# Kernel tuning notes

Hardware: AMD Instinct MI355X
Metric: run time of the kernel (lower is better)

Reference implementation:

```python
import jax, jax.numpy as jnp
import numpy as np

N_NODES = 50000
N_EDGES = 800000
HIDDEN = 64
DEPTH = 3
NUM_GRAPHS = 256
NUM_CLASSES = 1
BN_EPS = 1e-5


def setup_inputs() -> dict:
    key = jax.random.key(0)
    ks = jax.random.split(key, 12)
    x = jax.random.normal(ks[0], (N_NODES, HIDDEN), dtype=jnp.float32)
    edge_index = jax.random.randint(ks[1], (2, N_EDGES), 0, N_NODES, dtype=jnp.int32)
    batch = jnp.sort(jax.random.randint(ks[2], (N_NODES,), 0, NUM_GRAPHS, dtype=jnp.int32))
    s = 1.0 / np.sqrt(HIDDEN)
    W1 = jax.random.uniform(ks[3], (DEPTH, HIDDEN, HIDDEN), jnp.float32, -s, s)
    b1 = jax.random.uniform(ks[4], (DEPTH, HIDDEN), jnp.float32, -s, s)
    W2 = jax.random.uniform(ks[5], (DEPTH, HIDDEN, HIDDEN), jnp.float32, -s, s)
    b2 = jax.random.uniform(ks[6], (DEPTH, HIDDEN), jnp.float32, -s, s)
    gamma = jnp.ones((DEPTH, HIDDEN), jnp.float32)
    beta = jnp.zeros((DEPTH, HIDDEN), jnp.float32)
    Wf = jax.random.uniform(ks[7], (HIDDEN, NUM_CLASSES), jnp.float32, -s, s)
    bf = jax.random.uniform(ks[8], (NUM_CLASSES,), jnp.float32, -s, s)
    return {"x": x, "edge_index": edge_index, "batch": batch,
            "W1": W1, "b1": b1, "W2": W2, "b2": b2,
            "gamma": gamma, "beta": beta, "Wf": Wf, "bf": bf}


def reference(x, edge_index, batch, W1, b1, W2, b2, gamma, beta, Wf, bf):
    src, dst = edge_index[0], edge_index[1]
    for i in range(DEPTH):
        # GINConv: (1+eps)*x + scatter-add of neighbor features (eps=0)
        agg = jnp.zeros_like(x).at[dst].add(x[src])
        h = x + agg
        h = jax.nn.relu(h @ W1[i] + b1[i])
        h = jax.nn.relu(h @ W2[i] + b2[i])
        # BatchNorm over node dimension (training-mode batch stats)
        mean = h.mean(axis=0)
        var = ((h - mean) ** 2).mean(axis=0)
        h = (h - mean) * jax.lax.rsqrt(var + BN_EPS) * gamma[i] + beta[i]
        x = jax.nn.relu(h)
    pooled = jax.ops.segment_sum(x, batch, num_segments=NUM_GRAPHS)  # [G, H]
    return pooled @ Wf + bf
```

## Files before the change

kernel.cpp:

```cpp
#include <hip/hip_runtime.h>

#define HIDDEN_C 64
#define NCHUNK 256

typedef __attribute__((ext_vector_type(8))) short bf16x8;
typedef __attribute__((ext_vector_type(8))) unsigned short u16x8;
typedef __attribute__((ext_vector_type(4))) float f32x4;

__device__ __forceinline__ float4 f4zero() { return make_float4(0.f, 0.f, 0.f, 0.f); }

__device__ __forceinline__ unsigned short f2bf(float f) {
    unsigned u = __float_as_uint(f);
    u += 0x7FFF + ((u >> 16) & 1);
    return (unsigned short)(u >> 16);
}
__device__ __forceinline__ float bf2f(unsigned short h) {
    return __uint_as_float(((unsigned)h) << 16);
}

__device__ __forceinline__ int swz_idx(int row, int k) {
    return row * 64 + ((((k >> 3) ^ (row & 7)) << 3) | (k & 7));
}

__global__ __launch_bounds__(256) void k_blocksum(const int* __restrict__ deg,
                                                  int* __restrict__ partial, int n) {
    int base = blockIdx.x * 1024 + threadIdx.x * 4;
    int s = 0;
#pragma unroll
    for (int k = 0; k < 4; ++k) {
        int i = base + k;
        if (i < n) s += deg[i];
    }
    __shared__ int red[256];
    red[threadIdx.x] = s;
    __syncthreads();
    for (int d = 128; d > 0; d >>= 1) {
        if (threadIdx.x < d) red[threadIdx.x] += red[threadIdx.x + d];
        __syncthreads();
    }
    if (threadIdx.x == 0) partial[blockIdx.x] = red[0];
}

__global__ __launch_bounds__(256) void k_scanpartial(int* __restrict__ partial,
                                                     int* __restrict__ last_slot,
                                                     int nBlocks, int nE) {
    __shared__ int buf[256];
    int tid = threadIdx.x;
    int v = (tid < nBlocks) ? partial[tid] : 0;
    buf[tid] = v;
    __syncthreads();
    for (int d = 1; d < 256; d <<= 1) {
        int t = (tid >= d) ? buf[tid - d] : 0;
        __syncthreads();
        buf[tid] += t;
        __syncthreads();
    }
    if (tid < nBlocks) partial[tid] = buf[tid] - v;
    if (tid == 0) last_slot[0] = nE;
}

__global__ __launch_bounds__(256) void k_writeptr(const int* __restrict__ deg,
                                                  const int* __restrict__ partial,
                                                  int* __restrict__ outp, int n) {
    int tid = threadIdx.x;
    int base = blockIdx.x * 1024 + tid * 4;
    int d[4];
    int s = 0;
#pragma unroll
    for (int k = 0; k < 4; ++k) {
        int i = base + k;
        d[k] = (i < n) ? deg[i] : 0;
        s += d[k];
    }
    __shared__ int buf[256];
    buf[tid] = s;
    __syncthreads();
    for (int dd = 1; dd < 256; dd <<= 1) {
        int t = (tid >= dd) ? buf[tid - dd] : 0;
        __syncthreads();
        buf[tid] += t;
        __syncthreads();
    }
    int off = partial[blockIdx.x] + buf[tid] - s;
#pragma unroll
    for (int k = 0; k < 4; ++k) {
        int i = base + k;
        if (i < n) {
            outp[i] = off;
            off += d[k];
        }
    }
}

__global__ __launch_bounds__(256) void k_bcount(const int* __restrict__ dst,
                                                int* __restrict__ cnt,
                                                int nE, int chunkSz, int nBuckets) {
    __shared__ int h[1024];
    int c = blockIdx.x, tid = threadIdx.x;
    for (int i = tid; i < nBuckets; i += 256) h[i] = 0;
    __syncthreads();
    int beg = c * chunkSz;
    int end = beg + chunkSz; if (end > nE) end = nE;
    int e = beg + tid;
    for (; e + 256 < end; e += 512) {
        int d0 = dst[e];
        int d1 = dst[e + 256];
        atomicAdd(&h[d0 >> 6], 1);
        atomicAdd(&h[d1 >> 6], 1);
    }
    if (e < end) atomicAdd(&h[dst[e] >> 6], 1);
    __syncthreads();
    for (int i = tid; i < nBuckets; i += 256) cnt[i * NCHUNK + c] = h[i];
}

__global__ __launch_bounds__(256) void k_bscatter(const int* __restrict__ src,
                                                  const int* __restrict__ dst,
                                                  const int* __restrict__ eoff,
                                                  unsigned* __restrict__ ebuf,
                                                  int nE, int chunkSz, int nBuckets) {
    __shared__ int cur[1024];
    int c = blockIdx.x, tid = threadIdx.x;
    for (int i = tid; i < nBuckets; i += 256) cur[i] = eoff[i * NCHUNK + c];
    __syncthreads();
    int beg = c * chunkSz;
    int end = beg + chunkSz; if (end > nE) end = nE;
    int e = beg + tid;
    for (; e + 256 < end; e += 512) {
        int d0 = dst[e];
        int d1 = dst[e + 256];
        int s0 = src[e];
        int s1 = src[e + 256];
        int p0 = atomicAdd(&cur[d0 >> 6], 1);
        int p1 = atomicAdd(&cur[d1 >> 6], 1);
        ebuf[p0] = ((unsigned)(d0 & 63) << 16) | (unsigned)s0;
        ebuf[p1] = ((unsigned)(d1 & 63) << 16) | (unsigned)s1;
    }
    if (e < end) {
        int d = dst[e];
        int pos = atomicAdd(&cur[d >> 6], 1);
        ebuf[pos] = ((unsigned)(d & 63) << 16) | (unsigned)src[e];
    }
}

__global__ __launch_bounds__(256) void k_bfill(const unsigned* __restrict__ ebuf,
                                               const int* __restrict__ eoff,
                                               int* __restrict__ rowptr,
                                               int* __restrict__ col,
                                               int nNodes, int nE, int nBuckets) {
    __shared__ int deg[64], cur[64];
    int b = blockIdx.x, tid = threadIdx.x;
    int lo = eoff[b * NCHUNK];
    int hi = (b + 1 < nBuckets) ? eoff[(b + 1) * NCHUNK] : nE;
    if (tid < 64) deg[tid] = 0;
    __syncthreads();
    for (int e = lo + tid; e < hi; e += 256) atomicAdd(&deg[ebuf[e] >> 16], 1);
    __syncthreads();
    if (tid < 64) {
        int d = deg[tid];
        int s = d;
        for (int o = 1; o < 64; o <<= 1) {
            int t = __shfl_up(s, o, 64);
            if (tid >= o) s += t;
        }
        int st = s - d;
        cur[tid] = lo + st;
        int node = b * 64 + tid;
        if (node < nNodes) rowptr[node] = lo + st;
    }
    __syncthreads();
    for (int e = lo + tid; e < hi; e += 256) {
        unsigned pk = ebuf[e];
        int pos = atomicAdd(&cur[pk >> 16], 1);
        col[pos] = (int)(pk & 0xFFFFu);
    }
}

__global__ __launch_bounds__(256) void k_wprep(const float* __restrict__ W1,
                                               const float* __restrict__ W2,
                                               unsigned short* __restrict__ wt) {
    __shared__ unsigned short s[8192];
    int b = blockIdx.x;
    int layer = b >> 1;
    const float* src = ((b & 1) ? W2 : W1) + (size_t)layer * 4096;
    int tid = threadIdx.x;
    int k = tid >> 2;
    int f0 = (tid & 3) * 16;
    const float* srcp = src + k * 64 + f0;
#pragma unroll
    for (int j4 = 0; j4 < 4; ++j4) {
        float4 wv = *(const float4*)(srcp + j4 * 4);
        float c[4] = {wv.x, wv.y, wv.z, wv.w};
        int f = f0 + j4 * 4;
#pragma unroll
        for (int j = 0; j < 4; ++j) {
            unsigned short h = f2bf(c[j]);
            int ix = swz_idx(f + j, k);
            s[ix] = h;
            s[4096 + ix] = f2bf(c[j] - bf2f(h));
        }
    }
    __syncthreads();
    uint4* dst = (uint4*)(wt + (size_t)b * 8192);
    const uint4* sp = (const uint4*)s;
#pragma unroll
    for (int it = 0; it < 4; ++it) dst[it * 256 + tid] = sp[it * 256 + tid];
}

__global__ __launch_bounds__(256) void k_statred(const float* __restrict__ pstat,
                                                 float* __restrict__ stats, int nb) {
    int j = blockIdx.x;
    int tid = threadIdx.x;
    float s = 0.f;
    for (int b = tid; b < nb; b += 256) s += pstat[(size_t)b * 128 + j];
    __shared__ float red[256];
    red[tid] = s;
    __syncthreads();
    for (int d = 128; d > 0; d >>= 1) {
        if (tid < d) red[tid] += red[tid + d];
        __syncthreads();
    }
    if (tid == 0) stats[j] = red[0];
}

template <bool DOBN>
__global__ __launch_bounds__(256) void k_aggbn(const float4* __restrict__ x4,
                                               const int* __restrict__ rowptr,
                                               const int* __restrict__ col,
                                               const float* __restrict__ stats,
                                               const float* __restrict__ gamma,
                                               const float* __restrict__ beta,
                                               float4* __restrict__ h4,
                                               int nNodes, float invN) {
    int wid = threadIdx.x >> 6;
    int lane = threadIdx.x & 63;
    int grp = lane >> 4;
    int l16 = lane & 15;
    int n = blockIdx.x * 4 + wid;
    if (n >= nNodes) return;

    float4 sc = make_float4(1.f, 1.f, 1.f, 1.f);
    float4 sh = f4zero();
    if (DOBN) {
        float4 s  = ((const float4*)stats)[l16];
        float4 q  = ((const float4*)stats)[16 + l16];
        float4 ga = ((const float4*)gamma)[l16];
        float4 be = ((const float4*)beta)[l16];
        float m;
        m = s.x * invN; sc.x = ga.x * rsqrtf(q.x * invN - m * m + 1e-5f); sh.x = be.x - m * sc.x;
        m = s.y * invN; sc.y = ga.y * rsqrtf(q.y * invN - m * m + 1e-5f); sh.y = be.y - m * sc.y;
        m = s.z * invN; sc.z = ga.z * rsqrtf(q.z * invN - m * m + 1e-5f); sh.z = be.z - m * sc.z;
        m = s.w * invN; sc.w = ga.w * rsqrtf(q.w * invN - m * m + 1e-5f); sh.w = be.w - m * sc.w;
    }

    float4 acc = f4zero();
    {
        float4 v = x4[(size_t)n * 16 + l16];
        if (DOBN) {
            v.x = fmaxf(fmaf(v.x, sc.x, sh.x), 0.f);
            v.y = fmaxf(fmaf(v.y, sc.y, sh.y), 0.f);
            v.z = fmaxf(fmaf(v.z, sc.z, sh.z), 0.f);
            v.w = fmaxf(fmaf(v.w, sc.w, sh.w), 0.f);
        }
        if (grp == 0) acc = v;
    }

    int lo = rowptr[n], hi = rowptr[n + 1];
    int e = lo;
    for (; e + 8 <= hi; e += 8) {
        int i0 = col[e + grp];
        int i1 = col[e + 4 + grp];
        float4 v0 = x4[(size_t)i0 * 16 + l16];
        float4 v1 = x4[(size_t)i1 * 16 + l16];
        if (DOBN) {
            v0.x = fmaxf(fmaf(v0.x, sc.x, sh.x), 0.f);
            v0.y = fmaxf(fmaf(v0.y, sc.y, sh.y), 0.f);
            v0.z = fmaxf(fmaf(v0.z, sc.z, sh.z), 0.f);
            v0.w = fmaxf(fmaf(v0.w, sc.w, sh.w), 0.f);
            v1.x = fmaxf(fmaf(v1.x, sc.x, sh.x), 0.f);
            v1.y = fmaxf(fmaf(v1.y, sc.y, sh.y), 0.f);
            v1.z = fmaxf(fmaf(v1.z, sc.z, sh.z), 0.f);
            v1.w = fmaxf(fmaf(v1.w, sc.w, sh.w), 0.f);
        }
        acc.x += v0.x + v1.x; acc.y += v0.y + v1.y;
        acc.z += v0.z + v1.z; acc.w += v0.w + v1.w;
    }
    for (; e < hi; e += 4) {
        int ee = e + grp;
        bool ok = ee < hi;
        int idx = col[ok ? ee : (hi - 1)];
        float4 v = x4[(size_t)idx * 16 + l16];
        if (DOBN) {
            v.x = fmaxf(fmaf(v.x, sc.x, sh.x), 0.f);
            v.y = fmaxf(fmaf(v.y, sc.y, sh.y), 0.f);
            v.z = fmaxf(fmaf(v.z, sc.z, sh.z), 0.f);
            v.w = fmaxf(fmaf(v.w, sc.w, sh.w), 0.f);
        }
        if (ok) {
            acc.x += v.x; acc.y += v.y; acc.z += v.z; acc.w += v.w;
        }
    }

    acc.x += __shfl_xor(acc.x, 16, 64); acc.y += __shfl_xor(acc.y, 16, 64);
    acc.z += __shfl_xor(acc.z, 16, 64); acc.w += __shfl_xor(acc.w, 16, 64);
    acc.x += __shfl_xor(acc.x, 32, 64); acc.y += __shfl_xor(acc.y, 32, 64);
    acc.z += __shfl_xor(acc.z, 32, 64); acc.w += __shfl_xor(acc.w, 32, 64);

    if (lane < 16) h4[(size_t)n * 16 + l16] = acc;
}

__global__ __launch_bounds__(256, 5) void k_mlp(const float* __restrict__ h_in,
                                                float* __restrict__ h_out,
                                                const unsigned short* __restrict__ wt1,
                                                const float* __restrict__ b1,
                                                const unsigned short* __restrict__ wt2,
                                                const float* __restrict__ b2,
                                                float* __restrict__ pstat,
                                                int nNodes) {
    __shared__ __align__(16) unsigned short smem16[16384];
    unsigned short* sA_hi = smem16;
    unsigned short* sA_lo = smem16 + 4096;
    unsigned short* sW_hi = smem16 + 8192;
    unsigned short* sW_lo = smem16 + 12288;

    int tid = threadIdx.x;
    int n0 = blockIdx.x * 64;
    int lane = tid & 63;
    int w = tid >> 6;
    int lr = lane & 15;
    int q = lane >> 4;
    int r0 = w * 16;

    uint4 w2r[4];
#pragma unroll
    for (int it = 0; it < 4; ++it) w2r[it] = ((const uint4*)wt2)[it * 256 + tid];

#pragma unroll
    for (int it = 0; it < 2; ++it) {
        int idx = it * 256 + tid;
        int row = idx >> 3, ch = idx & 7;
        float4 v0 = f4zero(), v1 = f4zero();
        if (n0 + row < nNodes) {
            const float4* p = (const float4*)(h_in + (size_t)(n0 + row) * 64 + ch * 8);
            v0 = p[0]; v1 = p[1];
        }
        float f[8] = {v0.x, v0.y, v0.z, v0.w, v1.x, v1.y, v1.z, v1.w};
        u16x8 hv, lv;
#pragma unroll
        for (int j = 0; j < 8; ++j) {
            unsigned short h = f2bf(f[j]);
            hv[j] = h;
            lv[j] = f2bf(f[j] - bf2f(h));
        }
        int off = row * 64 + ((ch ^ (row & 7)) << 3);
        *(u16x8*)(sA_hi + off) = hv;
        *(u16x8*)(sA_lo + off) = lv;
    }
    {
        uint4* d = (uint4*)sW_hi;
        const uint4* s = (const uint4*)wt1;
#pragma unroll
        for (int it = 0; it < 4; ++it) d[it * 256 + tid] = s[it * 256 + tid];
    }
    __syncthreads();

    f32x4 acc[4];

#define GEMM_SPLIT(BIAS)                                                         \
    {                                                                            \
        int rowA = r0 + lr;                                                      \
        const unsigned short* pah = sA_hi + rowA * 64;                           \
        const unsigned short* pal = sA_lo + rowA * 64;                           \
        int sr = rowA & 7;                                                       \
        bf16x8 ah0 = *(const bf16x8*)(pah + ((q ^ sr) << 3));                    \
        bf16x8 ah1 = *(const bf16x8*)(pah + (((4 + q) ^ sr) << 3));              \
        bf16x8 al0 = *(const bf16x8*)(pal + ((q ^ sr) << 3));                    \
        bf16x8 al1 = *(const bf16x8*)(pal + (((4 + q) ^ sr) << 3));              \
        _Pragma("unroll")                                                        \
        for (int ct = 0; ct < 4; ++ct) {                                         \
            int f = ct * 16 + lr;                                                \
            const unsigned short* pbh = sW_hi + f * 64;                          \
            const unsigned short* pbl = sW_lo + f * 64;                          \
            int sf = f & 7;                                                      \
            bf16x8 bh0 = *(const bf16x8*)(pbh + ((q ^ sf) << 3));                \
            bf16x8 bh1 = *(const bf16x8*)(pbh + (((4 + q) ^ sf) << 3));          \
            bf16x8 bl0 = *(const bf16x8*)(pbl + ((q ^ sf) << 3));                \
            bf16x8 bl1 = *(const bf16x8*)(pbl + (((4 + q) ^ sf) << 3));          \
            float bias = BIAS[f];                                                \
            f32x4 c = {bias, bias, bias, bias};                                  \
            c = __builtin_amdgcn_mfma_f32_16x16x32_bf16(al0, bh0, c, 0, 0, 0);   \
            c = __builtin_amdgcn_mfma_f32_16x16x32_bf16(al1, bh1, c, 0, 0, 0);   \
            c = __builtin_amdgcn_mfma_f32_16x16x32_bf16(ah0, bl0, c, 0, 0, 0);   \
            c = __builtin_amdgcn_mfma_f32_16x16x32_bf16(ah1, bl1, c, 0, 0, 0);   \
            c = __builtin_amdgcn_mfma_f32_16x16x32_bf16(ah0, bh0, c, 0, 0, 0);   \
            c = __builtin_amdgcn_mfma_f32_16x16x32_bf16(ah1, bh1, c, 0, 0, 0);   \
            acc[ct] = c;                                                         \
        }                                                                        \
    }

    GEMM_SPLIT(b1)

    __syncthreads();

#pragma unroll
    for (int ct = 0; ct < 4; ++ct) {
        int f = ct * 16 + lr;
#pragma unroll
        for (int rg = 0; rg < 4; ++rg) {
            int row = r0 + q * 4 + rg;
            float v = fmaxf(acc[ct][rg], 0.f);
            unsigned short h = f2bf(v);
            int ix = swz_idx(row, f);
            sA_hi[ix] = h;
            sA_lo[ix] = f2bf(v - bf2f(h));
        }
    }
    {
        uint4* d = (uint4*)sW_hi;
#pragma unroll
        for (int it = 0; it < 4; ++it) d[it * 256 + tid] = w2r[it];
    }
    __syncthreads();

    GEMM_SPLIT(b2)

    __syncthreads();
#undef GEMM_SPLIT

    float* sS = (float*)sW_hi;
    float* sQ = sS + 256;

#pragma unroll
    for (int ct = 0; ct < 4; ++ct) {
        int f = ct * 16 + lr;
        float sp = 0.f, qp = 0.f;
#pragma unroll
        for (int rg = 0; rg < 4; ++rg) {
            int row = r0 + q * 4 + rg;
            float v = fmaxf(acc[ct][rg], 0.f);
            if (n0 + row < nNodes) {
                h_out[(size_t)(n0 + row) * 64 + f] = v;
                sp += v;
                qp += v * v;
            }
        }
        sp += __shfl_xor(sp, 16, 64); qp += __shfl_xor(qp, 16, 64);
        sp += __shfl_xor(sp, 32, 64); qp += __shfl_xor(qp, 32, 64);
        if (q == 0) {
            sS[w * 64 + f] = sp;
            sQ[w * 64 + f] = qp;
        }
    }
    __syncthreads();
    if (tid < 128) {
        float v;
        if (tid < 64)
            v = sS[tid] + sS[64 + tid] + sS[128 + tid] + sS[192 + tid];
        else {
            int f = tid - 64;
            v = sQ[f] + sQ[64 + f] + sQ[128 + f] + sQ[192 + f];
        }
        pstat[(size_t)blockIdx.x * 128 + tid] = v;
    }
}

__device__ __forceinline__ int lower_bound_dev(const int* a, int n, int key) {
    int lo = 0, hi = n;
    while (lo < hi) {
        int mid = (lo + hi) >> 1;
        if (a[mid] < key) lo = mid + 1; else hi = mid;
    }
    return lo;
}

__global__ __launch_bounds__(256) void k_pool(const float4* __restrict__ x4,
                                              const int* __restrict__ batch,
                                              const float* __restrict__ stats,
                                              const float* __restrict__ gamma,
                                              const float* __restrict__ beta,
                                              const float* __restrict__ Wf,
                                              const float* __restrict__ bf,
                                              float* __restrict__ out,
                                              int nNodes, float invN) {
    int wid = threadIdx.x >> 6;
    int lane = threadIdx.x & 63;
    int grp = lane >> 4;
    int l16 = lane & 15;
    int g = blockIdx.x * 4 + wid;

    float4 sc, sh;
    {
        float4 s  = ((const float4*)stats)[l16];
        float4 q  = ((const float4*)stats)[16 + l16];
        float4 ga = ((const float4*)gamma)[l16];
        float4 be = ((const float4*)beta)[l16];
        float m;
        m = s.x * invN; sc.x = ga.x * rsqrtf(q.x * invN - m * m + 1e-5f); sh.x = be.x - m * sc.x;
        m = s.y * invN; sc.y = ga.y * rsqrtf(q.y * invN - m * m + 1e-5f); sh.y = be.y - m * sc.y;
        m = s.z * invN; sc.z = ga.z * rsqrtf(q.z * invN - m * m + 1e-5f); sh.z = be.z - m * sc.z;
        m = s.w * invN; sc.w = ga.w * rsqrtf(q.w * invN - m * m + 1e-5f); sh.w = be.w - m * sc.w;
    }

    int lo = lower_bound_dev(batch, nNodes, g);
    int hi = lower_bound_dev(batch, nNodes, g + 1);

    float4 acc = f4zero();
    for (int r = lo + grp; r < hi; r += 4) {
        float4 v = x4[(size_t)r * 16 + l16];
        acc.x += fmaxf(fmaf(v.x, sc.x, sh.x), 0.f);
        acc.y += fmaxf(fmaf(v.y, sc.y, sh.y), 0.f);
        acc.z += fmaxf(fmaf(v.z, sc.z, sh.z), 0.f);
        acc.w += fmaxf(fmaf(v.w, sc.w, sh.w), 0.f);
    }
    acc.x += __shfl_xor(acc.x, 16, 64); acc.y += __shfl_xor(acc.y, 16, 64);
    acc.z += __shfl_xor(acc.z, 16, 64); acc.w += __shfl_xor(acc.w, 16, 64);
    acc.x += __shfl_xor(acc.x, 32, 64); acc.y += __shfl_xor(acc.y, 32, 64);
    acc.z += __shfl_xor(acc.z, 32, 64); acc.w += __shfl_xor(acc.w, 32, 64);

    float4 wf = ((const float4*)Wf)[l16];
    float p = acc.x * wf.x + acc.y * wf.y + acc.z * wf.z + acc.w * wf.w;
    p += __shfl_xor(p, 1, 64);
    p += __shfl_xor(p, 2, 64);
    p += __shfl_xor(p, 4, 64);
    p += __shfl_xor(p, 8, 64);
    if (lane == 0) out[g] = p + bf[0];
}

extern "C" void kernel_launch(void* const* d_in, const int* in_sizes, int n_in,
                              void* d_out, int out_size, void* d_ws, size_t ws_size,
                              hipStream_t stream) {
    const float* x_in  = (const float*)d_in[0];
    const int*   ei    = (const int*)d_in[1];
    const int*   batch = (const int*)d_in[2];
    const float* W1    = (const float*)d_in[3];
    const float* b1    = (const float*)d_in[4];
    const float* W2    = (const float*)d_in[5];
    const float* b2    = (const float*)d_in[6];
    const float* gamma = (const float*)d_in[7];
    const float* beta  = (const float*)d_in[8];
    const float* Wf    = (const float*)d_in[9];
    const float* bf    = (const float*)d_in[10];

    const int nNodes = in_sizes[0] / HIDDEN_C;
    const int nE = in_sizes[1] / 2;
    const int* src = ei;
    const int* dst = ei + nE;

    const int nBuckets = (nNodes + 63) / 64;
    const int nTot = nBuckets * NCHUNK;
    const int chunkSz = (nE + NCHUNK - 1) / NCHUNK;
    const int scanBlocks = (nTot + 1023) / 1024;
    const float invN = 1.f / (float)nNodes;

    const size_t NB = (size_t)nNodes * HIDDEN_C * sizeof(float);
    char* ws = (char*)d_ws;
    float*    bufA    = (float*)ws;
    float*    bufB    = (float*)(ws + NB);
    float*    stats   = (float*)(ws + 2 * NB);
    unsigned short* wtbuf = (unsigned short*)(ws + 2 * NB + 4096);
    float*    pstat   = (float*)(ws + 2 * NB + 4096 + 98304);
    int*      rowptr  = (int*)((char*)pstat + 409600);
    int*      partial = rowptr + nNodes + 64;
    int*      col     = partial + 256;
    unsigned* ebuf    = (unsigned*)bufB;
    int*      cnt     = (int*)((char*)bufB + (size_t)nE * 4);
    int*      eoff    = cnt + nTot + 64;

    const int mlpGrid = nBuckets;
    const int aggGrid = (nNodes + 3) / 4;

    k_wprep<<<6, 256, 0, stream>>>(W1, W2, wtbuf);
    k_bcount<<<NCHUNK, 256, 0, stream>>>(dst, cnt, nE, chunkSz, nBuckets);
    k_blocksum<<<scanBlocks, 256, 0, stream>>>(cnt, partial, nTot);
    k_scanpartial<<<1, 256, 0, stream>>>(partial, rowptr + nNodes, scanBlocks, nE);
    k_writeptr<<<scanBlocks, 256, 0, stream>>>(cnt, partial, eoff, nTot);
    k_bscatter<<<NCHUNK, 256, 0, stream>>>(src, dst, eoff, ebuf, nE, chunkSz, nBuckets);
    k_bfill<<<nBuckets, 256, 0, stream>>>(ebuf, eoff, rowptr, col, nNodes, nE, nBuckets);

    const float* prev_h = x_in;
    float* cur = bufA;
    for (int i = 0; i < 3; ++i) {
        if (i == 0) {
            k_aggbn<false><<<aggGrid, 256, 0, stream>>>((const float4*)prev_h, rowptr, col,
                                                        nullptr, nullptr, nullptr,
                                                        (float4*)cur, nNodes, invN);
        } else {
            k_aggbn<true><<<aggGrid, 256, 0, stream>>>((const float4*)prev_h, rowptr, col,
                                                       stats + (size_t)(i - 1) * 128,
                                                       gamma + (size_t)(i - 1) * 64,
                                                       beta + (size_t)(i - 1) * 64,
                                                       (float4*)cur, nNodes, invN);
        }
        k_mlp<<<mlpGrid, 256, 0, stream>>>(cur, cur,
                                           wtbuf + (size_t)(2 * i) * 8192, b1 + (size_t)i * 64,
                                           wtbuf + (size_t)(2 * i + 1) * 8192, b2 + (size_t)i * 64,
                                           pstat, nNodes);
        k_statred<<<128, 256, 0, stream>>>(pstat, stats + (size_t)i * 128, nBuckets);
        prev_h = cur;
        cur = (cur == bufA) ? bufB : bufA;
    }

    k_pool<<<64, 256, 0, stream>>>((const float4*)prev_h, batch,
                                   stats + 256, gamma + 128, beta + 128,
                                   Wf, bf, (float*)d_out, nNodes, invN);
}
```

Before: 212.8 us.

## Fuse neighbor aggregation and BN into the MLP kernel per layer

```diff
diff --git a/kernel.cpp b/kernel.cpp
--- a/kernel.cpp
+++ b/kernel.cpp
@@ -223,99 +223,19 @@
 }
 
 template <bool DOBN>
-__global__ __launch_bounds__(256) void k_aggbn(const float4* __restrict__ x4,
-                                               const int* __restrict__ rowptr,
-                                               const int* __restrict__ col,
-                                               const float* __restrict__ stats,
-                                               const float* __restrict__ gamma,
-                                               const float* __restrict__ beta,
-                                               float4* __restrict__ h4,
-                                               int nNodes, float invN) {
-    int wid = threadIdx.x >> 6;
-    int lane = threadIdx.x & 63;
-    int grp = lane >> 4;
-    int l16 = lane & 15;
-    int n = blockIdx.x * 4 + wid;
-    if (n >= nNodes) return;
-
-    float4 sc = make_float4(1.f, 1.f, 1.f, 1.f);
-    float4 sh = f4zero();
-    if (DOBN) {
-        float4 s  = ((const float4*)stats)[l16];
-        float4 q  = ((const float4*)stats)[16 + l16];
-        float4 ga = ((const float4*)gamma)[l16];
-        float4 be = ((const float4*)beta)[l16];
-        float m;
-        m = s.x * invN; sc.x = ga.x * rsqrtf(q.x * invN - m * m + 1e-5f); sh.x = be.x - m * sc.x;
-        m = s.y * invN; sc.y = ga.y * rsqrtf(q.y * invN - m * m + 1e-5f); sh.y = be.y - m * sc.y;
-        m = s.z * invN; sc.z = ga.z * rsqrtf(q.z * invN - m * m + 1e-5f); sh.z = be.z - m * sc.z;
-        m = s.w * invN; sc.w = ga.w * rsqrtf(q.w * invN - m * m + 1e-5f); sh.w = be.w - m * sc.w;
-    }
-
-    float4 acc = f4zero();
-    {
-        float4 v = x4[(size_t)n * 16 + l16];
-        if (DOBN) {
-            v.x = fmaxf(fmaf(v.x, sc.x, sh.x), 0.f);
-            v.y = fmaxf(fmaf(v.y, sc.y, sh.y), 0.f);
-            v.z = fmaxf(fmaf(v.z, sc.z, sh.z), 0.f);
-            v.w = fmaxf(fmaf(v.w, sc.w, sh.w), 0.f);
-        }
-        if (grp == 0) acc = v;
-    }
-
-    int lo = rowptr[n], hi = rowptr[n + 1];
-    int e = lo;
-    for (; e + 8 <= hi; e += 8) {
-        int i0 = col[e + grp];
-        int i1 = col[e + 4 + grp];
-        float4 v0 = x4[(size_t)i0 * 16 + l16];
-        float4 v1 = x4[(size_t)i1 * 16 + l16];
-        if (DOBN) {
-            v0.x = fmaxf(fmaf(v0.x, sc.x, sh.x), 0.f);
-            v0.y = fmaxf(fmaf(v0.y, sc.y, sh.y), 0.f);
-            v0.z = fmaxf(fmaf(v0.z, sc.z, sh.z), 0.f);
-            v0.w = fmaxf(fmaf(v0.w, sc.w, sh.w), 0.f);
-            v1.x = fmaxf(fmaf(v1.x, sc.x, sh.x), 0.f);
-            v1.y = fmaxf(fmaf(v1.y, sc.y, sh.y), 0.f);
-            v1.z = fmaxf(fmaf(v1.z, sc.z, sh.z), 0.f);
-            v1.w = fmaxf(fmaf(v1.w, sc.w, sh.w), 0.f);
-        }
-        acc.x += v0.x + v1.x; acc.y += v0.y + v1.y;
-        acc.z += v0.z + v1.z; acc.w += v0.w + v1.w;
-    }
-    for (; e < hi; e += 4) {
-        int ee = e + grp;
-        bool ok = ee < hi;
-        int idx = col[ok ? ee : (hi - 1)];
-        float4 v = x4[(size_t)idx * 16 + l16];
-        if (DOBN) {
-            v.x = fmaxf(fmaf(v.x, sc.x, sh.x), 0.f);
-            v.y = fmaxf(fmaf(v.y, sc.y, sh.y), 0.f);
-            v.z = fmaxf(fmaf(v.z, sc.z, sh.z), 0.f);
-            v.w = fmaxf(fmaf(v.w, sc.w, sh.w), 0.f);
-        }
-        if (ok) {
-            acc.x += v.x; acc.y += v.y; acc.z += v.z; acc.w += v.w;
-        }
-    }
-
-    acc.x += __shfl_xor(acc.x, 16, 64); acc.y += __shfl_xor(acc.y, 16, 64);
-    acc.z += __shfl_xor(acc.z, 16, 64); acc.w += __shfl_xor(acc.w, 16, 64);
-    acc.x += __shfl_xor(acc.x, 32, 64); acc.y += __shfl_xor(acc.y, 32, 64);
-    acc.z += __shfl_xor(acc.z, 32, 64); acc.w += __shfl_xor(acc.w, 32, 64);
-
-    if (lane < 16) h4[(size_t)n * 16 + l16] = acc;
-}
-
-__global__ __launch_bounds__(256, 5) void k_mlp(const float* __restrict__ h_in,
-                                                float* __restrict__ h_out,
-                                                const unsigned short* __restrict__ wt1,
-                                                const float* __restrict__ b1,
-                                                const unsigned short* __restrict__ wt2,
-                                                const float* __restrict__ b2,
-                                                float* __restrict__ pstat,
-                                                int nNodes) {
+__global__ __launch_bounds__(256, 5) void k_layer(const float4* __restrict__ x4,
+                                                  const int* __restrict__ rowptr,
+                                                  const int* __restrict__ col,
+                                                  const float* __restrict__ stats,
+                                                  const float* __restrict__ gamma,
+                                                  const float* __restrict__ beta,
+                                                  const unsigned short* __restrict__ wt1,
+                                                  const float* __restrict__ b1,
+                                                  const unsigned short* __restrict__ wt2,
+                                                  const float* __restrict__ b2,
+                                                  float* __restrict__ pstat,
+                                                  float* __restrict__ h_out,
+                                                  int nNodes, float invN) {
     __shared__ __align__(16) unsigned short smem16[16384];
     unsigned short* sA_hi = smem16;
     unsigned short* sA_lo = smem16 + 4096;
@@ -329,38 +249,92 @@
     int lr = lane & 15;
     int q = lane >> 4;
     int r0 = w * 16;
+    int grp = lane >> 4;
+    int l16 = lane & 15;
 
     uint4 w2r[4];
 #pragma unroll
     for (int it = 0; it < 4; ++it) w2r[it] = ((const uint4*)wt2)[it * 256 + tid];
 
-#pragma unroll
-    for (int it = 0; it < 2; ++it) {
-        int idx = it * 256 + tid;
-        int row = idx >> 3, ch = idx & 7;
-        float4 v0 = f4zero(), v1 = f4zero();
-        if (n0 + row < nNodes) {
-            const float4* p = (const float4*)(h_in + (size_t)(n0 + row) * 64 + ch * 8);
-            v0 = p[0]; v1 = p[1];
-        }
-        float f[8] = {v0.x, v0.y, v0.z, v0.w, v1.x, v1.y, v1.z, v1.w};
-        u16x8 hv, lv;
-#pragma unroll
-        for (int j = 0; j < 8; ++j) {
-            unsigned short h = f2bf(f[j]);
-            hv[j] = h;
-            lv[j] = f2bf(f[j] - bf2f(h));
-        }
-        int off = row * 64 + ((ch ^ (row & 7)) << 3);
-        *(u16x8*)(sA_hi + off) = hv;
-        *(u16x8*)(sA_lo + off) = lv;
-    }
     {
         uint4* d = (uint4*)sW_hi;
         const uint4* s = (const uint4*)wt1;
 #pragma unroll
         for (int it = 0; it < 4; ++it) d[it * 256 + tid] = s[it * 256 + tid];
     }
+
+    float4 sc = make_float4(1.f, 1.f, 1.f, 1.f);
+    float4 sh = f4zero();
+    if (DOBN) {
+        float4 s  = ((const float4*)stats)[l16];
+        float4 qv = ((const float4*)stats)[16 + l16];
+        float4 ga = ((const float4*)gamma)[l16];
+        float4 be = ((const float4*)beta)[l16];
+        float m;
+        m = s.x * invN; sc.x = ga.x * rsqrtf(qv.x * invN - m * m + 1e-5f); sh.x = be.x - m * sc.x;
+        m = s.y * invN; sc.y = ga.y * rsqrtf(qv.y * invN - m * m + 1e-5f); sh.y = be.y - m * sc.y;
+        m = s.z * invN; sc.z = ga.z * rsqrtf(qv.z * invN - m * m + 1e-5f); sh.z = be.z - m * sc.z;
+        m = s.w * invN; sc.w = ga.w * rsqrtf(qv.w * invN - m * m + 1e-5f); sh.w = be.w - m * sc.w;
+    }
+
+#define APPLYBN(V)                                          \
+    if (DOBN) {                                             \
+        V.x = fmaxf(fmaf(V.x, sc.x, sh.x), 0.f);            \
+        V.y = fmaxf(fmaf(V.y, sc.y, sh.y), 0.f);            \
+        V.z = fmaxf(fmaf(V.z, sc.z, sh.z), 0.f);            \
+        V.w = fmaxf(fmaf(V.w, sc.w, sh.w), 0.f);            \
+    }
+
+    for (int i = 0; i < 16; ++i) {
+        int rloc = r0 + i;
+        int n = n0 + rloc;
+        float4 acc = f4zero();
+        if (n < nNodes) {
+            if (grp == 0) {
+                float4 v = x4[(size_t)n * 16 + l16];
+                APPLYBN(v)
+                acc = v;
+            }
+            int lo = rowptr[n], hi = rowptr[n + 1];
+            int e = lo;
+            for (; e + 8 <= hi; e += 8) {
+                int i0 = col[e + grp];
+                int i1 = col[e + 4 + grp];
+                float4 v0 = x4[(size_t)i0 * 16 + l16];
+                float4 v1 = x4[(size_t)i1 * 16 + l16];
+                APPLYBN(v0)
+                APPLYBN(v1)
+                acc.x += v0.x + v1.x; acc.y += v0.y + v1.y;
+                acc.z += v0.z + v1.z; acc.w += v0.w + v1.w;
+            }
+            for (; e < hi; e += 4) {
+                int ee = e + grp;
+                bool ok = ee < hi;
+                int idx = col[ok ? ee : (hi - 1)];
+                float4 v = x4[(size_t)idx * 16 + l16];
+                APPLYBN(v)
+                if (ok) {
+                    acc.x += v.x; acc.y += v.y; acc.z += v.z; acc.w += v.w;
+                }
+            }
+        }
+        acc.x += __shfl_xor(acc.x, 16, 64); acc.y += __shfl_xor(acc.y, 16, 64);
+        acc.z += __shfl_xor(acc.z, 16, 64); acc.w += __shfl_xor(acc.w, 16, 64);
+        acc.x += __shfl_xor(acc.x, 32, 64); acc.y += __shfl_xor(acc.y, 32, 64);
+        acc.z += __shfl_xor(acc.z, 32, 64); acc.w += __shfl_xor(acc.w, 32, 64);
+
+        if (lane < 16) {
+            ushort4 hv, lv;
+            hv.x = f2bf(acc.x); lv.x = f2bf(acc.x - bf2f(hv.x));
+            hv.y = f2bf(acc.y); lv.y = f2bf(acc.y - bf2f(hv.y));
+            hv.z = f2bf(acc.z); lv.z = f2bf(acc.z - bf2f(hv.z));
+            hv.w = f2bf(acc.w); lv.w = f2bf(acc.w - bf2f(hv.w));
+            int ix = rloc * 64 + ((((l16 >> 1) ^ (rloc & 7)) << 3) | ((l16 & 1) << 2));
+            *(ushort4*)(sA_hi + ix) = hv;
+            *(ushort4*)(sA_lo + ix) = lv;
+        }
+    }
+#undef APPLYBN
     __syncthreads();
 
     f32x4 acc[4];
@@ -565,8 +539,7 @@
     int*      cnt     = (int*)((char*)bufB + (size_t)nE * 4);
     int*      eoff    = cnt + nTot + 64;
 
-    const int mlpGrid = nBuckets;
-    const int aggGrid = (nNodes + 3) / 4;
+    const int layerGrid = nBuckets;
 
     k_wprep<<<6, 256, 0, stream>>>(W1, W2, wtbuf);
     k_bcount<<<NCHUNK, 256, 0, stream>>>(dst, cnt, nE, chunkSz, nBuckets);
@@ -580,20 +553,17 @@
     float* cur = bufA;
     for (int i = 0; i < 3; ++i) {
         if (i == 0) {
-            k_aggbn<false><<<aggGrid, 256, 0, stream>>>((const float4*)prev_h, rowptr, col,
-                                                        nullptr, nullptr, nullptr,
-                                                        (float4*)cur, nNodes, invN);
+            k_layer<false><<<layerGrid, 256, 0, stream>>>((const float4*)prev_h, rowptr, col,
+                nullptr, nullptr, nullptr,
+                wtbuf, b1, wtbuf + 8192, b2,
+                pstat, cur, nNodes, invN);
         } else {
-            k_aggbn<true><<<aggGrid, 256, 0, stream>>>((const float4*)prev_h, rowptr, col,
-                                                       stats + (size_t)(i - 1) * 128,
-                                                       gamma + (size_t)(i - 1) * 64,
-                                                       beta + (size_t)(i - 1) * 64,
-                                                       (float4*)cur, nNodes, invN);
-        }
-        k_mlp<<<mlpGrid, 256, 0, stream>>>(cur, cur,
-                                           wtbuf + (size_t)(2 * i) * 8192, b1 + (size_t)i * 64,
-                                           wtbuf + (size_t)(2 * i + 1) * 8192, b2 + (size_t)i * 64,
-                                           pstat, nNodes);
+            k_layer<true><<<layerGrid, 256, 0, stream>>>((const float4*)prev_h, rowptr, col,
+                stats + (size_t)(i - 1) * 128, gamma + (size_t)(i - 1) * 64, beta + (size_t)(i - 1) * 64,
+                wtbuf + (size_t)(2 * i) * 8192, b1 + (size_t)i * 64,
+                wtbuf + (size_t)(2 * i + 1) * 8192, b2 + (size_t)i * 64,
+                pstat, cur, nNodes, invN);
+        }
         k_statred<<<128, 256, 0, stream>>>(pstat, stats + (size_t)i * 128, nBuckets);
         prev_h = cur;
         cur = (cur == bufA) ? bufB : bufA;
```

Result: slower. 251.7 us (+18.3%).

## Store node feature buffers in fp16 to halve gather and stream bandwidth

Applied to the files above, without the earlier changes.

```diff
diff --git a/kernel.cpp b/kernel.cpp
--- a/kernel.cpp
+++ b/kernel.cpp
@@ -17,9 +17,31 @@
 __device__ __forceinline__ float bf2f(unsigned short h) {
     return __uint_as_float(((unsigned)h) << 16);
 }
+__device__ __forceinline__ unsigned short f2h(float f) {
+    _Float16 h = (_Float16)f;
+    unsigned short u;
+    __builtin_memcpy(&u, &h, 2);
+    return u;
+}
+__device__ __forceinline__ float h2f(unsigned short u) {
+    _Float16 h;
+    __builtin_memcpy(&h, &u, 2);
+    return (float)h;
+}
 
 __device__ __forceinline__ int swz_idx(int row, int k) {
     return row * 64 + ((((k >> 3) ^ (row & 7)) << 3) | (k & 7));
+}
+
+__global__ __launch_bounds__(256) void k_xcvt(const float4* __restrict__ in,
+                                              ushort4* __restrict__ out, int n4) {
+    int i = blockIdx.x * 256 + threadIdx.x;
+    if (i < n4) {
+        float4 v = in[i];
+        ushort4 o;
+        o.x = f2h(v.x); o.y = f2h(v.y); o.z = f2h(v.z); o.w = f2h(v.w);
+        out[i] = o;
+    }
 }
 
 __global__ __launch_bounds__(256) void k_blocksum(const int* __restrict__ deg,
@@ -223,13 +245,13 @@
 }
 
 template <bool DOBN>
-__global__ __launch_bounds__(256) void k_aggbn(const float4* __restrict__ x4,
+__global__ __launch_bounds__(256) void k_aggbn(const unsigned short* __restrict__ x16,
                                                const int* __restrict__ rowptr,
                                                const int* __restrict__ col,
                                                const float* __restrict__ stats,
                                                const float* __restrict__ gamma,
                                                const float* __restrict__ beta,
-                                               float4* __restrict__ h4,
+                                               unsigned short* __restrict__ hout,
                                                int nNodes, float invN) {
     int wid = threadIdx.x >> 6;
     int lane = threadIdx.x & 63;
@@ -252,15 +274,22 @@
         m = s.w * invN; sc.w = ga.w * rsqrtf(q.w * invN - m * m + 1e-5f); sh.w = be.w - m * sc.w;
     }
 
+#define LOADROW(IDX, V)                                                      \
+    {                                                                        \
+        ushort4 uv = *(const ushort4*)(x16 + (size_t)(IDX) * 64 + l16 * 4);  \
+        V.x = h2f(uv.x); V.y = h2f(uv.y); V.z = h2f(uv.z); V.w = h2f(uv.w);  \
+        if (DOBN) {                                                          \
+            V.x = fmaxf(fmaf(V.x, sc.x, sh.x), 0.f);                         \
+            V.y = fmaxf(fmaf(V.y, sc.y, sh.y), 0.f);                         \
+            V.z = fmaxf(fmaf(V.z, sc.z, sh.z), 0.f);                         \
+            V.w = fmaxf(fmaf(V.w, sc.w, sh.w), 0.f);                         \
+        }                                                                    \
+    }
+
     float4 acc = f4zero();
     {
-        float4 v = x4[(size_t)n * 16 + l16];
-        if (DOBN) {
-            v.x = fmaxf(fmaf(v.x, sc.x, sh.x), 0.f);
-            v.y = fmaxf(fmaf(v.y, sc.y, sh.y), 0.f);
-            v.z = fmaxf(fmaf(v.z, sc.z, sh.z), 0.f);
-            v.w = fmaxf(fmaf(v.w, sc.w, sh.w), 0.f);
-        }
+        float4 v;
+        LOADROW(n, v)
         if (grp == 0) acc = v;
     }
 
@@ -269,18 +298,9 @@
     for (; e + 8 <= hi; e += 8) {
         int i0 = col[e + grp];
         int i1 = col[e + 4 + grp];
-        float4 v0 = x4[(size_t)i0 * 16 + l16];
-        float4 v1 = x4[(size_t)i1 * 16 + l16];
-        if (DOBN) {
-            v0.x = fmaxf(fmaf(v0.x, sc.x, sh.x), 0.f);
-            v0.y = fmaxf(fmaf(v0.y, sc.y, sh.y), 0.f);
-            v0.z = fmaxf(fmaf(v0.z, sc.z, sh.z), 0.f);
-            v0.w = fmaxf(fmaf(v0.w, sc.w, sh.w), 0.f);
-            v1.x = fmaxf(fmaf(v1.x, sc.x, sh.x), 0.f);
-            v1.y = fmaxf(fmaf(v1.y, sc.y, sh.y), 0.f);
-            v1.z = fmaxf(fmaf(v1.z, sc.z, sh.z), 0.f);
-            v1.w = fmaxf(fmaf(v1.w, sc.w, sh.w), 0.f);
-        }
+        float4 v0, v1;
+        LOADROW(i0, v0)
+        LOADROW(i1, v1)
         acc.x += v0.x + v1.x; acc.y += v0.y + v1.y;
         acc.z += v0.z + v1.z; acc.w += v0.w + v1.w;
     }
@@ -288,28 +308,28 @@
         int ee = e + grp;
         bool ok = ee < hi;
         int idx = col[ok ? ee : (hi - 1)];
-        float4 v = x4[(size_t)idx * 16 + l16];
-        if (DOBN) {
-            v.x = fmaxf(fmaf(v.x, sc.x, sh.x), 0.f);
-            v.y = fmaxf(fmaf(v.y, sc.y, sh.y), 0.f);
-            v.z = fmaxf(fmaf(v.z, sc.z, sh.z), 0.f);
-            v.w = fmaxf(fmaf(v.w, sc.w, sh.w), 0.f);
-        }
+        float4 v;
+        LOADROW(idx, v)
         if (ok) {
             acc.x += v.x; acc.y += v.y; acc.z += v.z; acc.w += v.w;
         }
     }
+#undef LOADROW
 
     acc.x += __shfl_xor(acc.x, 16, 64); acc.y += __shfl_xor(acc.y, 16, 64);
     acc.z += __shfl_xor(acc.z, 16, 64); acc.w += __shfl_xor(acc.w, 16, 64);
     acc.x += __shfl_xor(acc.x, 32, 64); acc.y += __shfl_xor(acc.y, 32, 64);
     acc.z += __shfl_xor(acc.z, 32, 64); acc.w += __shfl_xor(acc.w, 32, 64);
 
-    if (lane < 16) h4[(size_t)n * 16 + l16] = acc;
-}
-
-__global__ __launch_bounds__(256, 5) void k_mlp(const float* __restrict__ h_in,
-                                                float* __restrict__ h_out,
+    if (lane < 16) {
+        ushort4 o;
+        o.x = f2h(acc.x); o.y = f2h(acc.y); o.z = f2h(acc.z); o.w = f2h(acc.w);
+        *(ushort4*)(hout + (size_t)n * 64 + l16 * 4) = o;
+    }
+}
+
+__global__ __launch_bounds__(256, 5) void k_mlp(const unsigned short* __restrict__ h_in,
+                                                unsigned short* __restrict__ h_out,
                                                 const unsigned short* __restrict__ wt1,
                                                 const float* __restrict__ b1,
                                                 const unsigned short* __restrict__ wt2,
@@ -338,18 +358,16 @@
     for (int it = 0; it < 2; ++it) {
         int idx = it * 256 + tid;
         int row = idx >> 3, ch = idx & 7;
-        float4 v0 = f4zero(), v1 = f4zero();
-        if (n0 + row < nNodes) {
-            const float4* p = (const float4*)(h_in + (size_t)(n0 + row) * 64 + ch * 8);
-            v0 = p[0]; v1 = p[1];
-        }
-        float f[8] = {v0.x, v0.y, v0.z, v0.w, v1.x, v1.y, v1.z, v1.w};
+        u16x8 iv = (u16x8)(0);
+        if (n0 + row < nNodes)
+            iv = *(const u16x8*)(h_in + (size_t)(n0 + row) * 64 + ch * 8);
         u16x8 hv, lv;
 #pragma unroll
         for (int j = 0; j < 8; ++j) {
-            unsigned short h = f2bf(f[j]);
+            float f = h2f(iv[j]);
+            unsigned short h = f2bf(f);
             hv[j] = h;
-            lv[j] = f2bf(f[j] - bf2f(h));
+            lv[j] = f2bf(f - bf2f(h));
         }
         int off = row * 64 + ((ch ^ (row & 7)) << 3);
         *(u16x8*)(sA_hi + off) = hv;
@@ -438,9 +456,11 @@
             int row = r0 + q * 4 + rg;
             float v = fmaxf(acc[ct][rg], 0.f);
             if (n0 + row < nNodes) {
-                h_out[(size_t)(n0 + row) * 64 + f] = v;
-                sp += v;
-                qp += v * v;
+                unsigned short hv = f2h(v);
+                h_out[(size_t)(n0 + row) * 64 + f] = hv;
+                float vq = h2f(hv);
+                sp += vq;
+                qp += vq * vq;
             }
         }
         sp += __shfl_xor(sp, 16, 64); qp += __shfl_xor(qp, 16, 64);
@@ -472,7 +492,7 @@
     return lo;
 }
 
-__global__ __launch_bounds__(256) void k_pool(const float4* __restrict__ x4,
+__global__ __launch_bounds__(256) void k_pool(const unsigned short* __restrict__ x16,
                                               const int* __restrict__ batch,
                                               const float* __restrict__ stats,
                                               const float* __restrict__ gamma,
@@ -505,11 +525,11 @@
 
     float4 acc = f4zero();
     for (int r = lo + grp; r < hi; r += 4) {
-        float4 v = x4[(size_t)r * 16 + l16];
-        acc.x += fmaxf(fmaf(v.x, sc.x, sh.x), 0.f);
-        acc.y += fmaxf(fmaf(v.y, sc.y, sh.y), 0.f);
-        acc.z += fmaxf(fmaf(v.z, sc.z, sh.z), 0.f);
-        acc.w += fmaxf(fmaf(v.w, sc.w, sh.w), 0.f);
+        ushort4 uv = *(const ushort4*)(x16 + (size_t)r * 64 + l16 * 4);
+        acc.x += fmaxf(fmaf(h2f(uv.x), sc.x, sh.x), 0.f);
+        acc.y += fmaxf(fmaf(h2f(uv.y), sc.y, sh.y), 0.f);
+        acc.z += fmaxf(fmaf(h2f(uv.z), sc.z, sh.z), 0.f);
+        acc.w += fmaxf(fmaf(h2f(uv.w), sc.w, sh.w), 0.f);
     }
     acc.x += __shfl_xor(acc.x, 16, 64); acc.y += __shfl_xor(acc.y, 16, 64);
     acc.z += __shfl_xor(acc.z, 16, 64); acc.w += __shfl_xor(acc.w, 16, 64);
@@ -551,23 +571,26 @@
     const int scanBlocks = (nTot + 1023) / 1024;
     const float invN = 1.f / (float)nNodes;
 
-    const size_t NB = (size_t)nNodes * HIDDEN_C * sizeof(float);
+    const size_t NH = ((size_t)nNodes * HIDDEN_C * sizeof(unsigned short) + 255) & ~(size_t)255;
     char* ws = (char*)d_ws;
-    float*    bufA    = (float*)ws;
-    float*    bufB    = (float*)(ws + NB);
-    float*    stats   = (float*)(ws + 2 * NB);
-    unsigned short* wtbuf = (unsigned short*)(ws + 2 * NB + 4096);
-    float*    pstat   = (float*)(ws + 2 * NB + 4096 + 98304);
+    unsigned short* x16 = (unsigned short*)ws;
+    unsigned short* hA  = (unsigned short*)(ws + NH);
+    unsigned short* hB  = (unsigned short*)(ws + 2 * NH);
+    float*    stats   = (float*)(ws + 3 * NH);
+    unsigned short* wtbuf = (unsigned short*)(ws + 3 * NH + 4096);
+    float*    pstat   = (float*)(ws + 3 * NH + 4096 + 98304);
     int*      rowptr  = (int*)((char*)pstat + 409600);
     int*      partial = rowptr + nNodes + 64;
     int*      col     = partial + 256;
-    unsigned* ebuf    = (unsigned*)bufB;
-    int*      cnt     = (int*)((char*)bufB + (size_t)nE * 4);
+    unsigned* ebuf    = (unsigned*)hB;
+    int*      cnt     = (int*)((char*)hB + (size_t)nE * 4);
     int*      eoff    = cnt + nTot + 64;
 
     const int mlpGrid = nBuckets;
     const int aggGrid = (nNodes + 3) / 4;
-
+    const int cvtGrid = (nNodes * 16 + 255) / 256;
+
+    k_xcvt<<<cvtGrid, 256, 0, stream>>>((const float4*)x_in, (ushort4*)x16, nNodes * 16);
     k_wprep<<<6, 256, 0, stream>>>(W1, W2, wtbuf);
     k_bcount<<<NCHUNK, 256, 0, stream>>>(dst, cnt, nE, chunkSz, nBuckets);
     k_blocksum<<<scanBlocks, 256, 0, stream>>>(cnt, partial, nTot);
@@ -576,19 +599,19 @@
     k_bscatter<<<NCHUNK, 256, 0, stream>>>(src, dst, eoff, ebuf, nE, chunkSz, nBuckets);
     k_bfill<<<nBuckets, 256, 0, stream>>>(ebuf, eoff, rowptr, col, nNodes, nE, nBuckets);
 
-    const float* prev_h = x_in;
-    float* cur = bufA;
+    const unsigned short* prev_h = x16;
+    unsigned short* cur = hA;
     for (int i = 0; i < 3; ++i) {
         if (i == 0) {
-            k_aggbn<false><<<aggGrid, 256, 0, stream>>>((const float4*)prev_h, rowptr, col,
+            k_aggbn<false><<<aggGrid, 256, 0, stream>>>(prev_h, rowptr, col,
                                                         nullptr, nullptr, nullptr,
-                                                        (float4*)cur, nNodes, invN);
+                                                        cur, nNodes, invN);
         } else {
-            k_aggbn<true><<<aggGrid, 256, 0, stream>>>((const float4*)prev_h, rowptr, col,
+            k_aggbn<true><<<aggGrid, 256, 0, stream>>>(prev_h, rowptr, col,
                                                        stats + (size_t)(i - 1) * 128,
                                                        gamma + (size_t)(i - 1) * 64,
                                                        beta + (size_t)(i - 1) * 64,
-                                                       (float4*)cur, nNodes, invN);
+                                                       cur, nNodes, invN);
         }
         k_mlp<<<mlpGrid, 256, 0, stream>>>(cur, cur,
                                            wtbuf + (size_t)(2 * i) * 8192, b1 + (size_t)i * 64,
@@ -596,10 +619,9 @@
                                            pstat, nNodes);
         k_statred<<<128, 256, 0, stream>>>(pstat, stats + (size_t)i * 128, nBuckets);
         prev_h = cur;
-        cur = (cur == bufA) ? bufB : bufA;
-    }
-
-    k_pool<<<64, 256, 0, stream>>>((const float4*)prev_h, batch,
-                                   stats + 256, gamma + 128, beta + 128,
+        cur = (cur == hA) ? hB : hA;
+    }
+
+    k_pool<<<64, 256, 0, stream>>>(prev_h, batch, stats + 256, gamma + 128, beta + 128,
                                    Wf, bf, (float*)d_out, nNodes, invN);
 }
```

Result: faster. 201.9 us (-5.1%).
